# Performance work log

Hardware: AMD Instinct MI355X
Metric: run time of the kernel (lower is better)

The kernel has to match this reference:

```python
import jax, jax.numpy as jnp
import numpy as np

B, C, H, W = 4, 256, 64, 64
CI = 128  # inter_channels = in_channels // 2
EPS = 1e-5  # torch BatchNorm default eps


def setup_inputs() -> dict:
    key = jax.random.key(0)
    ks = jax.random.split(key, 8)

    def w(k, shape, s=0.02):
        return jax.random.normal(k, shape, jnp.float32) * s

    return {
        "x": jax.random.normal(ks[0], (B, C, H, W), jnp.float32),
        # theta (Q) linear + BatchNorm1d (inference-mode running stats)
        "theta_w": w(ks[1], (CI, C)), "theta_b": jnp.zeros((CI,), jnp.float32),
        "theta_bn_gamma": jnp.ones((CI,), jnp.float32), "theta_bn_beta": jnp.zeros((CI,), jnp.float32),
        "theta_bn_mean": jnp.zeros((CI,), jnp.float32), "theta_bn_var": jnp.ones((CI,), jnp.float32),
        # phi (K) linear + BatchNorm1d
        "phi_w": w(ks[2], (CI, C)), "phi_b": jnp.zeros((CI,), jnp.float32),
        "phi_bn_gamma": jnp.ones((CI,), jnp.float32), "phi_bn_beta": jnp.zeros((CI,), jnp.float32),
        "phi_bn_mean": jnp.zeros((CI,), jnp.float32), "phi_bn_var": jnp.ones((CI,), jnp.float32),
        # g (V) linear
        "g_w": w(ks[3], (CI, C)), "g_b": jnp.zeros((CI,), jnp.float32),
        # W_z output linear
        "wz_w": w(ks[4], (C, CI)), "wz_b": jnp.zeros((C,), jnp.float32),
        # output BatchNorm2d (gamma nonzero instead of init-0 so output is non-trivial)
        "bn_gamma": w(ks[5], (C,), 0.1), "bn_beta": jnp.zeros((C,), jnp.float32),
        "bn_mean": jnp.zeros((C,), jnp.float32), "bn_var": jnp.ones((C,), jnp.float32),
    }


def _linear(z, w, b):
    # z: [B, N, C], w: [D, C] -> [B, N, D]
    return jnp.einsum('bnc,dc->bnd', z, w) + b


def _bn(z, gamma, beta, mean, var):
    # per-channel affine BN in inference mode, channel on last axis
    return (z - mean) * jax.lax.rsqrt(var + EPS) * gamma + beta


def reference(x, theta_w, theta_b, theta_bn_gamma, theta_bn_beta, theta_bn_mean, theta_bn_var,
              phi_w, phi_b, phi_bn_gamma, phi_bn_beta, phi_bn_mean, phi_bn_var,
              g_w, g_b, wz_w, wz_b, bn_gamma, bn_beta, bn_mean, bn_var):
    b, c, h, w = x.shape
    n = h * w
    ci = theta_w.shape[0]
    scale = float(ci) ** (-0.5)

    x_flat = x.reshape(b, c, n).transpose(0, 2, 1)  # [B, N, C]
    Q = _bn(_linear(x_flat, theta_w, theta_b), theta_bn_gamma, theta_bn_beta, theta_bn_mean, theta_bn_var)
    K = _bn(_linear(x_flat, phi_w, phi_b), phi_bn_gamma, phi_bn_beta, phi_bn_mean, phi_bn_var)
    V = _linear(x_flat, g_w, g_b)  # [B, N, CI]

    # attention computed in fp32 (matches torch amp-disabled block)
    attn = jnp.einsum('bnd,bmd->bnm', Q.astype(jnp.float32), K.astype(jnp.float32)) * scale
    attn = jax.nn.softmax(attn, axis=-1).astype(V.dtype)  # [B, N, N]

    y = jnp.einsum('bnm,bmd->bnd', attn, V)  # [B, N, CI]
    y = jnp.einsum('bnd,cd->bnc', y, wz_w) + wz_b  # [B, N, C]
    y = y.transpose(0, 2, 1).reshape(b, c, h, w)

    # BatchNorm2d (inference mode), channel axis 1
    rstd = jax.lax.rsqrt(bn_var + EPS)
    y = (y - bn_mean[None, :, None, None]) * (rstd * bn_gamma)[None, :, None, None] + bn_beta[None, :, None, None]
    return y + x
```

## Files before the change

kernel.cpp:

```cpp
#include <hip/hip_runtime.h>
#include <stdint.h>

typedef __attribute__((ext_vector_type(8))) short bf16x8;
typedef __attribute__((ext_vector_type(4))) float f32x4;
typedef __attribute__((ext_vector_type(16))) float f32x16;
typedef __attribute__((ext_vector_type(2))) unsigned int uint2v;

#define WS_WQKV   0u
#define WS_WZ     196608u
#define WS_SCL    262144u
#define WS_SHF    263680u
#define WS_WZS    265216u
#define WS_WZT    266240u
#define WS_Q      524288u
#define WS_K      (WS_Q  + 4194304u)
#define WS_VT     (WS_K  + 4194304u)
#define WS_Y      (WS_VT + 4194304u)
#define WS_OP     (WS_Y  + 4194304u)
#define WS_LP     (WS_OP + 16777216u)

__device__ __forceinline__ short f2bf(float f) {
  union { float f; uint32_t u; } v; v.f = f;
  uint32_t r = v.u + 0x7fffu + ((v.u >> 16) & 1u);
  return (short)(r >> 16);
}

__device__ __forceinline__ uint32_t pack2_bf16(float a, float b) {
  union { float f; uint32_t u; } x, y; x.f = a; y.f = b;
  return ((y.u + 0x8000u) & 0xffff0000u) | ((x.u + 0x8000u) >> 16);
}

__device__ __forceinline__ f32x4 mfma16(bf16x8 a, bf16x8 b, f32x4 c) {
  return __builtin_amdgcn_mfma_f32_16x16x32_bf16(a, b, c, 0, 0, 0);
}
__device__ __forceinline__ f32x16 mfma32(bf16x8 a, bf16x8 b, f32x16 c) {
  return __builtin_amdgcn_mfma_f32_32x32x16_bf16(a, b, c, 0, 0, 0);
}

__device__ __forceinline__ void load_lds16(const short* gp, short* lp) {
  __builtin_amdgcn_global_load_lds(
      (const __attribute__((address_space(1))) uint32_t*)gp,
      (__attribute__((address_space(3))) uint32_t*)lp, 16, 0, 0);
}

__global__ __launch_bounds__(256) void prep_kernel(
    const float* theta_w, const float* phi_w, const float* g_w, const float* wz_w,
    const float* theta_b, const float* tg, const float* tb, const float* tm, const float* tv,
    const float* phi_b,   const float* pg, const float* pb, const float* pm, const float* pv,
    const float* g_b,
    const float* wz_b, const float* bg, const float* bb, const float* bm, const float* bv,
    char* ws) {
  int idx = blockIdx.x * 256 + threadIdx.x;
  short* wqkv = (short*)(ws + WS_WQKV);
  if (idx < 98304) {
    float w;
    if (idx < 32768) w = theta_w[idx];
    else if (idx < 65536) w = phi_w[idx - 32768];
    else w = g_w[idx - 65536];
    wqkv[idx] = f2bf(w);
  }
  if (idx < 32768) ((short*)(ws + WS_WZ))[idx] = f2bf(wz_w[idx]);
  if (idx < 384) {
    float s, t;
    if (idx < 128)      { s = tg[idx] * rsqrtf(tv[idx] + 1e-5f);
                          t = (theta_b[idx] - tm[idx]) * s + tb[idx]; }
    else if (idx < 256) { int d = idx - 128; s = pg[d] * rsqrtf(pv[d] + 1e-5f);
                          t = (phi_b[d] - pm[d]) * s + pb[d]; }
    else                { int d = idx - 256; s = 1.0f; t = g_b[d]; }
    ((float*)(ws + WS_SCL))[idx] = s;
    ((float*)(ws + WS_SHF))[idx] = t;
  }
  if (idx < 256) {
    float s = bg[idx] * rsqrtf(bv[idx] + 1e-5f);
    float t = (wz_b[idx] - bm[idx]) * s + bb[idx];
    ((float*)(ws + WS_WZS))[idx] = s;
    ((float*)(ws + WS_WZT))[idx] = t;
  }
}

__global__ __launch_bounds__(256) void qkv_kernel(const float* __restrict__ x, char* ws) {
  const int nt2 = blockIdx.x, b = blockIdx.y;
  const int t = threadIdx.x;
  __shared__ __attribute__((aligned(16))) short xs[16][264];
  const short* wqkv = (const short*)(ws + WS_WQKV);
  const float* scl = (const float*)(ws + WS_SCL);
  const float* shf = (const float*)(ws + WS_SHF);
  const int n0 = nt2 * 16;
  #pragma unroll
  for (int i = 0; i < 4; ++i) {
    int chunk = i * 256 + t;
    int c = chunk >> 2, n4 = chunk & 3;
    const float4 v = *(const float4*)(x + ((size_t)(b * 256 + c) << 12) + n0 + n4 * 4);
    xs[n4 * 4 + 0][c] = f2bf(v.x);
    xs[n4 * 4 + 1][c] = f2bf(v.y);
    xs[n4 * 4 + 2][c] = f2bf(v.z);
    xs[n4 * 4 + 3][c] = f2bf(v.w);
  }
  __syncthreads();
  const int wv = t >> 6, l = t & 63, lr = l & 15, q = l >> 4;
  bf16x8 a[8];
  #pragma unroll
  for (int kt = 0; kt < 8; ++kt) a[kt] = *(const bf16x8*)&xs[lr][kt * 32 + q * 8];
  f32x4 acc[6] = {};
  #pragma unroll
  for (int kt = 0; kt < 8; ++kt) {
    #pragma unroll
    for (int s = 0; s < 6; ++s) {
      const short* wp = wqkv + (size_t)(wv * 96 + s * 16 + lr) * 256 + kt * 32 + q * 8;
      bf16x8 bf = *(const bf16x8*)wp;
      if (wv * 96 + s * 16 < 256) acc[s] = mfma16(bf, a[kt], acc[s]);
      else                        acc[s] = mfma16(a[kt], bf, acc[s]);
    }
  }
  const float s2 = 0.08838834764831845f * 1.4426950408889634f;
  short* Qp = (short*)(ws + WS_Q)  + ((size_t)b << 19);
  short* Kt = (short*)(ws + WS_K)  + ((size_t)b << 19);
  short* Vt = (short*)(ws + WS_VT) + ((size_t)b << 19);
  #pragma unroll
  for (int s = 0; s < 6; ++s) {
    int dgb = wv * 96 + s * 16;
    if (dgb < 256) {
      const int n = n0 + lr;
      const int d4 = dgb + q * 4;
      short4 pk;
      {
        short vals[4];
        #pragma unroll
        for (int r = 0; r < 4; ++r) {
          int dg = d4 + r;
          float sc = scl[dg], sh = shf[dg];
          if (dgb < 128) { sc *= s2; sh *= s2; }
          vals[r] = f2bf(acc[s][r] * sc + sh);
        }
        pk.x = vals[0]; pk.y = vals[1]; pk.z = vals[2]; pk.w = vals[3];
      }
      if (dgb < 128) {
        *(short4*)(Qp + (size_t)n * 128 + d4) = pk;
      } else {
        int c4 = d4 - 128;
        int tile = n >> 6, nn = n & 63;
        int mb = nn >> 5, rr = nn & 31;
        int ks = c4 >> 4, h = (c4 >> 3) & 1, e0 = c4 & 7;
        size_t base = (size_t)tile * 8192 + (size_t)(mb * 8 + ks) * 512
                    + (size_t)(h * 32 + rr) * 8 + e0;
        *(short4*)(Kt + base) = pk;
      }
    } else {
      int dg = dgb + lr;
      float sc = scl[dg], sh = shf[dg];
      short4 pk;
      pk.x = f2bf(acc[s][0] * sc + sh);
      pk.y = f2bf(acc[s][1] * sc + sh);
      pk.z = f2bf(acc[s][2] * sc + sh);
      pk.w = f2bf(acc[s][3] * sc + sh);
      int d = dg - 256;
      int nbase = n0 + q * 4;
      int tile = nbase >> 6, nn = nbase & 63;
      int dt = d >> 5, rv = d & 31;
      int ks2 = nn >> 4, hv = (nn >> 3) & 1, e0 = nn & 7;
      size_t base = (size_t)tile * 8192 + (size_t)(dt * 4 + ks2) * 512
                  + (size_t)(hv * 32 + rv) * 8 + e0;
      *(short4*)(Vt + base) = pk;
    }
  }
}

__global__ __launch_bounds__(256, 2) void attn_kernel(char* ws) {
  const int g = blockIdx.x;
  const int b = (g & 7) >> 1;
  const int idx = ((g >> 3) << 1) | (g & 1);
  const int nt = idx >> 2, mc = idx & 3;
  const int t = threadIdx.x, w = t >> 6, l = t & 63;
  const int lq = l & 31, h = l >> 5;
  __shared__ __attribute__((aligned(16))) short ks0[16][512];
  __shared__ __attribute__((aligned(16))) short vs0[16][512];
  __shared__ __attribute__((aligned(16))) short ks1[16][512];
  __shared__ __attribute__((aligned(16))) short vs1[16][512];
  const short* Q  = (const short*)(ws + WS_Q)  + ((size_t)b << 19);
  const short* Kt = (const short*)(ws + WS_K)  + ((size_t)b << 19);
  const short* Vt = (const short*)(ws + WS_VT) + ((size_t)b << 19);
  const int n0w = nt * 128 + w * 32;
  bf16x8 qf[8];
  #pragma unroll
  for (int ks = 0; ks < 8; ++ks)
    qf[ks] = *(const bf16x8*)(Q + (size_t)(n0w + lq) * 128 + ks * 16 + h * 8);
  f32x16 o[4] = {};
  float lsum = 0.f;

  const short* kbase = Kt + (size_t)(mc * 16) * 8192;
  const short* vbase = Vt + (size_t)(mc * 16) * 8192;

  auto stage = [&](short (*KS)[512], short (*VS)[512], int it) {
    const short* kg = kbase + (size_t)it * 8192;
    const short* vg = vbase + (size_t)it * 8192;
    #pragma unroll
    for (int i = 0; i < 4; ++i) {
      int gi = i * 4 + w;
      load_lds16(kg + gi * 512 + l * 8, &KS[gi][0]);
      load_lds16(vg + gi * 512 + l * 8, &VS[gi][0]);
    }
  };

  auto compute = [&](short (*ksl)[512], short (*vsl)[512]) {
    f32x16 sacc[2] = {};
    __builtin_amdgcn_s_setprio(1);
    #pragma unroll
    for (int ks = 0; ks < 8; ++ks) {
      #pragma unroll
      for (int mb = 0; mb < 2; ++mb) {
        bf16x8 kf = *(const bf16x8*)&ksl[mb * 8 + ks][l * 8];
        sacc[mb] = mfma32(kf, qf[ks], sacc[mb]);
      }
    }
    __builtin_amdgcn_s_setprio(0);
    bf16x8 pf[4];
    #pragma unroll
    for (int mb = 0; mb < 2; ++mb) {
      float e[16];
      #pragma unroll
      for (int r = 0; r < 16; ++r) {
        e[r] = exp2f(sacc[mb][r]);
        lsum += e[r];
      }
      #pragma unroll
      for (int k = 0; k < 2; ++k) {
        uint32_t va0 = pack2_bf16(e[8 * k + 0], e[8 * k + 1]);
        uint32_t va1 = pack2_bf16(e[8 * k + 2], e[8 * k + 3]);
        uint32_t vb0 = pack2_bf16(e[8 * k + 4], e[8 * k + 5]);
        uint32_t vb1 = pack2_bf16(e[8 * k + 6], e[8 * k + 7]);
        uint2v s0 = __builtin_amdgcn_permlane32_swap(va0, vb0, false, false);
        uint2v s1 = __builtin_amdgcn_permlane32_swap(va1, vb1, false, false);
        union { uint32_t u[4]; bf16x8 v; } pk;
        pk.u[0] = s0[0]; pk.u[1] = s1[0]; pk.u[2] = s0[1]; pk.u[3] = s1[1];
        pf[2 * mb + k] = pk.v;
      }
    }
    __builtin_amdgcn_s_setprio(1);
    #pragma unroll
    for (int dt = 0; dt < 4; ++dt) {
      #pragma unroll
      for (int ks2 = 0; ks2 < 4; ++ks2) {
        bf16x8 vf = *(const bf16x8*)&vsl[dt * 4 + ks2][l * 8];
        o[dt] = mfma32(vf, pf[ks2], o[dt]);
      }
    }
    __builtin_amdgcn_s_setprio(0);
  };

  stage(ks0, vs0, 0);
  __syncthreads();
  for (int it2 = 0; it2 < 8; ++it2) {
    stage(ks1, vs1, it2 * 2 + 1);
    compute(ks0, vs0);
    __syncthreads();
    if (it2 < 7) stage(ks0, vs0, it2 * 2 + 2);
    compute(ks1, vs1);
    __syncthreads();
  }

  const int cb = mc * 4 + b;
  float* LP = (float*)(ws + WS_LP) + ((size_t)cb << 12);
  {
    float s = lsum;
    s += __shfl_xor(s, 32, 64);
    if (l < 32) LP[n0w + l] = s;
  }
  short* OPc = (short*)(ws + WS_OP) + ((size_t)cb << 19);
  #pragma unroll
  for (int dt = 0; dt < 4; ++dt) {
    #pragma unroll
    for (int rg = 0; rg < 4; ++rg) {
      short4 pk;
      pk.x = f2bf(o[dt][rg * 4 + 0]);
      pk.y = f2bf(o[dt][rg * 4 + 1]);
      pk.z = f2bf(o[dt][rg * 4 + 2]);
      pk.w = f2bf(o[dt][rg * 4 + 3]);
      *(short4*)&OPc[((size_t)(n0w + lq) << 7) + dt * 32 + rg * 8 + h * 4] = pk;
    }
  }
}

__global__ __launch_bounds__(256) void proj_kernel(const float* __restrict__ x,
                                                   char* ws, float* __restrict__ out) {
  const int nt = blockIdx.x, b = blockIdx.y;
  const int t = threadIdx.x, wv = t >> 6, l = t & 63, lr = l & 15, q = l >> 4;
  __shared__ __attribute__((aligned(16))) short ys[16][136];
  const short* OP = (const short*)(ws + WS_OP);
  const float* LP = (const float*)(ws + WS_LP);
  const short* WZ = (const short*)(ws + WS_WZ);
  const float* wzs = (const float*)(ws + WS_WZS);
  const float* wzt = (const float*)(ws + WS_WZT);
  const int n0 = nt * 16;
  {
    int row = t >> 4, d8 = (t & 15) * 8;
    int n = n0 + row;
    float acc8[8] = {};
    float lsf = 0.f;
    #pragma unroll
    for (int mc = 0; mc < 4; ++mc) {
      int cb = mc * 4 + b;
      const short* p = OP + ((size_t)cb << 19) + ((size_t)n << 7) + d8;
      uint4 v = *(const uint4*)p;
      uint32_t uu[4] = {v.x, v.y, v.z, v.w};
      #pragma unroll
      for (int w = 0; w < 4; ++w) {
        union { uint32_t u; float f; } lo, hi;
        lo.u = uu[w] << 16; hi.u = uu[w] & 0xffff0000u;
        acc8[w * 2 + 0] += lo.f;
        acc8[w * 2 + 1] += hi.f;
      }
      lsf += LP[(cb << 12) + n];
    }
    float inv = 1.0f / lsf;
    short out8[8];
    #pragma unroll
    for (int j = 0; j < 8; ++j) out8[j] = f2bf(acc8[j] * inv);
    *(uint4*)&ys[row][d8] = *(uint4*)out8;
  }
  __syncthreads();
  bf16x8 a[4];
  #pragma unroll
  for (int kt = 0; kt < 4; ++kt) a[kt] = *(const bf16x8*)&ys[lr][kt * 32 + q * 8];
  f32x4 acc[4] = {};
  #pragma unroll
  for (int kt = 0; kt < 4; ++kt) {
    #pragma unroll
    for (int s = 0; s < 4; ++s) {
      const short* wp = WZ + (size_t)(wv * 64 + s * 16 + lr) * 128 + kt * 32 + q * 8;
      bf16x8 bf = *(const bf16x8*)wp;
      acc[s] = mfma16(a[kt], bf, acc[s]);
    }
  }
  #pragma unroll
  for (int s = 0; s < 4; ++s) {
    int c = wv * 64 + s * 16 + lr;
    float sc = wzs[c], sh = wzt[c];
    int nbase = n0 + q * 4;
    size_t base = ((size_t)(b * 256 + c) << 12) + nbase;
    float4 xv = *(const float4*)(x + base);
    float4 ov;
    ov.x = acc[s][0] * sc + sh + xv.x;
    ov.y = acc[s][1] * sc + sh + xv.y;
    ov.z = acc[s][2] * sc + sh + xv.z;
    ov.w = acc[s][3] * sc + sh + xv.w;
    *(float4*)(out + base) = ov;
  }
}

extern "C" void kernel_launch(void* const* d_in, const int* in_sizes, int n_in,
                              void* d_out, int out_size, void* d_ws, size_t ws_size,
                              hipStream_t stream) {
  const float* x       = (const float*)d_in[0];
  const float* theta_w = (const float*)d_in[1];
  const float* theta_b = (const float*)d_in[2];
  const float* tg      = (const float*)d_in[3];
  const float* tb      = (const float*)d_in[4];
  const float* tm      = (const float*)d_in[5];
  const float* tv      = (const float*)d_in[6];
  const float* phi_w   = (const float*)d_in[7];
  const float* phi_b   = (const float*)d_in[8];
  const float* pg      = (const float*)d_in[9];
  const float* pb      = (const float*)d_in[10];
  const float* pm      = (const float*)d_in[11];
  const float* pv      = (const float*)d_in[12];
  const float* g_w     = (const float*)d_in[13];
  const float* g_b     = (const float*)d_in[14];
  const float* wz_w    = (const float*)d_in[15];
  const float* wz_b    = (const float*)d_in[16];
  const float* bg      = (const float*)d_in[17];
  const float* bb      = (const float*)d_in[18];
  const float* bm      = (const float*)d_in[19];
  const float* bv      = (const float*)d_in[20];
  char* ws = (char*)d_ws;
  float* out = (float*)d_out;

  prep_kernel<<<384, 256, 0, stream>>>(theta_w, phi_w, g_w, wz_w,
                                       theta_b, tg, tb, tm, tv,
                                       phi_b, pg, pb, pm, pv,
                                       g_b, wz_b, bg, bb, bm, bv, ws);
  qkv_kernel<<<dim3(256, 4), 256, 0, stream>>>(x, ws);
  attn_kernel<<<512, 256, 0, stream>>>(ws);
  proj_kernel<<<dim3(256, 4), 256, 0, stream>>>(x, ws, out);
}
```

Measured before the change: 200.6 us.

## Load K/V fragments directly from global into registers, dropping LDS double buffering

The attention kernel no longer stages K and V tiles into double-buffered shared memory with async global-to-LDS loads and block barriers. Each wave now loads its own K and V bf16 fragments straight from global memory (through L2) into registers every iteration. This removes the LDS traffic and the __syncthreads, but every wave in the block now fetches the same K/V data separately, and there is no longer explicit prefetch overlap across iterations. Register pressure rises with 32 extra bf16x8 fragments held per thread.

```diff
diff --git a/kernel.cpp b/kernel.cpp
--- a/kernel.cpp
+++ b/kernel.cpp
@@ -35,12 +35,6 @@
 }
 __device__ __forceinline__ f32x16 mfma32(bf16x8 a, bf16x8 b, f32x16 c) {
   return __builtin_amdgcn_mfma_f32_32x32x16_bf16(a, b, c, 0, 0, 0);
-}
-
-__device__ __forceinline__ void load_lds16(const short* gp, short* lp) {
-  __builtin_amdgcn_global_load_lds(
-      (const __attribute__((address_space(1))) uint32_t*)gp,
-      (__attribute__((address_space(3))) uint32_t*)lp, 16, 0, 0);
 }
 
 __global__ __launch_bounds__(256) void prep_kernel(
@@ -172,10 +166,6 @@
   const int nt = idx >> 2, mc = idx & 3;
   const int t = threadIdx.x, w = t >> 6, l = t & 63;
   const int lq = l & 31, h = l >> 5;
-  __shared__ __attribute__((aligned(16))) short ks0[16][512];
-  __shared__ __attribute__((aligned(16))) short vs0[16][512];
-  __shared__ __attribute__((aligned(16))) short ks1[16][512];
-  __shared__ __attribute__((aligned(16))) short vs1[16][512];
   const short* Q  = (const short*)(ws + WS_Q)  + ((size_t)b << 19);
   const short* Kt = (const short*)(ws + WS_K)  + ((size_t)b << 19);
   const short* Vt = (const short*)(ws + WS_VT) + ((size_t)b << 19);
@@ -187,32 +177,27 @@
   f32x16 o[4] = {};
   float lsum = 0.f;
 
-  const short* kbase = Kt + (size_t)(mc * 16) * 8192;
-  const short* vbase = Vt + (size_t)(mc * 16) * 8192;
-
-  auto stage = [&](short (*KS)[512], short (*VS)[512], int it) {
+  const short* kbase = Kt + (size_t)(mc * 16) * 8192 + l * 8;
+  const short* vbase = Vt + (size_t)(mc * 16) * 8192 + l * 8;
+
+  for (int it = 0; it < 16; ++it) {
     const short* kg = kbase + (size_t)it * 8192;
     const short* vg = vbase + (size_t)it * 8192;
-    #pragma unroll
-    for (int i = 0; i < 4; ++i) {
-      int gi = i * 4 + w;
-      load_lds16(kg + gi * 512 + l * 8, &KS[gi][0]);
-      load_lds16(vg + gi * 512 + l * 8, &VS[gi][0]);
-    }
-  };
-
-  auto compute = [&](short (*ksl)[512], short (*vsl)[512]) {
+    bf16x8 kf[16];
+    #pragma unroll
+    for (int gi = 0; gi < 16; ++gi) kf[gi] = *(const bf16x8*)(kg + gi * 512);
     f32x16 sacc[2] = {};
     __builtin_amdgcn_s_setprio(1);
     #pragma unroll
     for (int ks = 0; ks < 8; ++ks) {
       #pragma unroll
-      for (int mb = 0; mb < 2; ++mb) {
-        bf16x8 kf = *(const bf16x8*)&ksl[mb * 8 + ks][l * 8];
-        sacc[mb] = mfma32(kf, qf[ks], sacc[mb]);
-      }
+      for (int mb = 0; mb < 2; ++mb)
+        sacc[mb] = mfma32(kf[mb * 8 + ks], qf[ks], sacc[mb]);
     }
     __builtin_amdgcn_s_setprio(0);
+    bf16x8 vf[16];
+    #pragma unroll
+    for (int gi = 0; gi < 16; ++gi) vf[gi] = *(const bf16x8*)(vg + gi * 512);
     bf16x8 pf[4];
     #pragma unroll
     for (int mb = 0; mb < 2; ++mb) {
@@ -239,23 +224,10 @@
     #pragma unroll
     for (int dt = 0; dt < 4; ++dt) {
       #pragma unroll
-      for (int ks2 = 0; ks2 < 4; ++ks2) {
-        bf16x8 vf = *(const bf16x8*)&vsl[dt * 4 + ks2][l * 8];
-        o[dt] = mfma32(vf, pf[ks2], o[dt]);
-      }
+      for (int ks2 = 0; ks2 < 4; ++ks2)
+        o[dt] = mfma32(vf[dt * 4 + ks2], pf[ks2], o[dt]);
     }
     __builtin_amdgcn_s_setprio(0);
-  };
-
-  stage(ks0, vs0, 0);
-  __syncthreads();
-  for (int it2 = 0; it2 < 8; ++it2) {
-    stage(ks1, vs1, it2 * 2 + 1);
-    compute(ks0, vs0);
-    __syncthreads();
-    if (it2 < 7) stage(ks0, vs0, it2 * 2 + 2);
-    compute(ks1, vs1);
-    __syncthreads();
   }
 
   const int cb = mc * 4 + b;
```

After: 206.8 us. +3.1%, slower.

## Split attention output dims across two blocks and drop LDS double buffering

Applied to the files above, without the earlier changes.

Each attention block now handles only half of the V head dimension, so the grid doubles to 1024 blocks. The QK^T scores and exp are recomputed in both halves. LDS use is cut by removing the double buffer and halving the V tile, and launch bounds are raised to 4 blocks per CU to increase occupancy. In exchange, the QK^T MFMA work is duplicated and global-to-LDS loads are no longer overlapped with compute within a block.

```diff
diff --git a/kernel.cpp b/kernel.cpp
--- a/kernel.cpp
+++ b/kernel.cpp
@@ -165,17 +165,17 @@
   }
 }
 
-__global__ __launch_bounds__(256, 2) void attn_kernel(char* ws) {
+__global__ __launch_bounds__(256, 4) void attn_kernel(char* ws) {
   const int g = blockIdx.x;
   const int b = (g & 7) >> 1;
   const int idx = ((g >> 3) << 1) | (g & 1);
-  const int nt = idx >> 2, mc = idx & 3;
+  const int nt = idx >> 3;
+  const int mc = (idx >> 1) & 3;
+  const int dh = idx & 1;
   const int t = threadIdx.x, w = t >> 6, l = t & 63;
   const int lq = l & 31, h = l >> 5;
-  __shared__ __attribute__((aligned(16))) short ks0[16][512];
-  __shared__ __attribute__((aligned(16))) short vs0[16][512];
-  __shared__ __attribute__((aligned(16))) short ks1[16][512];
-  __shared__ __attribute__((aligned(16))) short vs1[16][512];
+  __shared__ __attribute__((aligned(16))) short ksl[16][512];
+  __shared__ __attribute__((aligned(16))) short vsl[8][512];
   const short* Q  = (const short*)(ws + WS_Q)  + ((size_t)b << 19);
   const short* Kt = (const short*)(ws + WS_K)  + ((size_t)b << 19);
   const short* Vt = (const short*)(ws + WS_VT) + ((size_t)b << 19);
@@ -184,24 +184,29 @@
   #pragma unroll
   for (int ks = 0; ks < 8; ++ks)
     qf[ks] = *(const bf16x8*)(Q + (size_t)(n0w + lq) * 128 + ks * 16 + h * 8);
-  f32x16 o[4] = {};
+  f32x16 o[2] = {};
   float lsum = 0.f;
 
   const short* kbase = Kt + (size_t)(mc * 16) * 8192;
-  const short* vbase = Vt + (size_t)(mc * 16) * 8192;
-
-  auto stage = [&](short (*KS)[512], short (*VS)[512], int it) {
-    const short* kg = kbase + (size_t)it * 8192;
-    const short* vg = vbase + (size_t)it * 8192;
-    #pragma unroll
-    for (int i = 0; i < 4; ++i) {
-      int gi = i * 4 + w;
-      load_lds16(kg + gi * 512 + l * 8, &KS[gi][0]);
-      load_lds16(vg + gi * 512 + l * 8, &VS[gi][0]);
-    }
-  };
-
-  auto compute = [&](short (*ksl)[512], short (*vsl)[512]) {
+  const short* vbase = Vt + (size_t)(mc * 16) * 8192 + (size_t)(dh * 8) * 512;
+
+  for (int it = 0; it < 16; ++it) {
+    __syncthreads();
+    {
+      const short* kg = kbase + (size_t)it * 8192;
+      const short* vg = vbase + (size_t)it * 8192;
+      #pragma unroll
+      for (int i = 0; i < 4; ++i) {
+        int gi = w * 4 + i;
+        load_lds16(kg + gi * 512 + l * 8, &ksl[gi][0]);
+      }
+      #pragma unroll
+      for (int i = 0; i < 2; ++i) {
+        int gi = w * 2 + i;
+        load_lds16(vg + gi * 512 + l * 8, &vsl[gi][0]);
+      }
+    }
+    __syncthreads();
     f32x16 sacc[2] = {};
     __builtin_amdgcn_s_setprio(1);
     #pragma unroll
@@ -237,44 +242,34 @@
     }
     __builtin_amdgcn_s_setprio(1);
     #pragma unroll
-    for (int dt = 0; dt < 4; ++dt) {
+    for (int dtl = 0; dtl < 2; ++dtl) {
       #pragma unroll
       for (int ks2 = 0; ks2 < 4; ++ks2) {
-        bf16x8 vf = *(const bf16x8*)&vsl[dt * 4 + ks2][l * 8];
-        o[dt] = mfma32(vf, pf[ks2], o[dt]);
+        bf16x8 vf = *(const bf16x8*)&vsl[dtl * 4 + ks2][l * 8];
+        o[dtl] = mfma32(vf, pf[ks2], o[dtl]);
       }
     }
     __builtin_amdgcn_s_setprio(0);
-  };
-
-  stage(ks0, vs0, 0);
-  __syncthreads();
-  for (int it2 = 0; it2 < 8; ++it2) {
-    stage(ks1, vs1, it2 * 2 + 1);
-    compute(ks0, vs0);
-    __syncthreads();
-    if (it2 < 7) stage(ks0, vs0, it2 * 2 + 2);
-    compute(ks1, vs1);
-    __syncthreads();
   }
 
   const int cb = mc * 4 + b;
-  float* LP = (float*)(ws + WS_LP) + ((size_t)cb << 12);
-  {
+  if (dh == 0) {
+    float* LP = (float*)(ws + WS_LP) + ((size_t)cb << 12);
     float s = lsum;
     s += __shfl_xor(s, 32, 64);
     if (l < 32) LP[n0w + l] = s;
   }
   short* OPc = (short*)(ws + WS_OP) + ((size_t)cb << 19);
   #pragma unroll
-  for (int dt = 0; dt < 4; ++dt) {
+  for (int dtl = 0; dtl < 2; ++dtl) {
+    const int dt = dh * 2 + dtl;
     #pragma unroll
     for (int rg = 0; rg < 4; ++rg) {
       short4 pk;
-      pk.x = f2bf(o[dt][rg * 4 + 0]);
-      pk.y = f2bf(o[dt][rg * 4 + 1]);
-      pk.z = f2bf(o[dt][rg * 4 + 2]);
-      pk.w = f2bf(o[dt][rg * 4 + 3]);
+      pk.x = f2bf(o[dtl][rg * 4 + 0]);
+      pk.y = f2bf(o[dtl][rg * 4 + 1]);
+      pk.z = f2bf(o[dtl][rg * 4 + 2]);
+      pk.w = f2bf(o[dtl][rg * 4 + 3]);
       *(short4*)&OPc[((size_t)(n0w + lq) << 7) + dt * 32 + rg * 8 + h * 4] = pk;
     }
   }
@@ -379,6 +374,6 @@
                                        phi_b, pg, pb, pm, pv,
                                        g_b, wz_b, bg, bb, bm, bv, ws);
   qkv_kernel<<<dim3(256, 4), 256, 0, stream>>>(x, ws);
-  attn_kernel<<<512, 256, 0, stream>>>(ws);
+  attn_kernel<<<1024, 256, 0, stream>>>(ws);
   proj_kernel<<<dim3(256, 4), 256, 0, stream>>>(x, ws, out);
 }
```

Result: slower. 221.8 us (+10.6%).
